# Performance work log

Measured on AMD Instinct MI355X. Metric: run time of the kernel, lower is better.

The kernel has to match this reference:

```python
import jax, jax.numpy as jnp
import numpy as np

R_MAX = 32
S_MAX = 2
N_RES_BINS = 2 * R_MAX + 2      # 66 (shared by residue and token one-hots)
N_CHAIN_BINS = 2 * S_MAX + 2    # 6
NO_BINS = N_RES_BINS + N_RES_BINS + 1 + N_CHAIN_BINS  # 139
C_Z = 128


def setup_inputs() -> dict:
    key = jax.random.key(0)
    ks = jax.random.split(key, 6)
    B, N = 1, 1024
    asym_id = jax.random.randint(ks[0], (B, N), 0, 8, dtype=jnp.int32)
    residue_index = jnp.sort(jax.random.randint(ks[1], (B, N), 0, 1024, dtype=jnp.int32), axis=-1)
    entity_id = jax.random.randint(ks[2], (B, N), 0, 4, dtype=jnp.int32)
    token_index = jnp.sort(jax.random.randint(ks[3], (B, N), 0, 2048, dtype=jnp.int32), axis=-1)
    sym_id = jax.random.randint(ks[4], (B, N), 0, 4, dtype=jnp.int32)
    # Linear(no_bins, c_z, bias=False): weight shape [c_z, no_bins]
    W = jax.random.normal(ks[5], (C_Z, NO_BINS), dtype=jnp.float32) * (NO_BINS ** -0.5)
    return {
        "asym_id": asym_id,
        "residue_index": residue_index,
        "entity_id": entity_id,
        "token_index": token_index,
        "sym_id": sym_id,
        "W": W,
    }


def _rel_feat(asym_id, residue_index, entity_id, token_index, sym_id, dtype=jnp.float32):
    # pairwise [B, N, N] comparisons
    b_same_chain = asym_id[..., :, None] == asym_id[..., None, :]
    b_same_residue = residue_index[..., :, None] == residue_index[..., None, :]
    b_same_entity = entity_id[..., :, None] == entity_id[..., None, :]

    # residue-level relative position, clamped; off-chain -> sentinel bin 2*r_max+1
    d_residue = residue_index[..., :, None] - residue_index[..., None, :]
    d_residue = jnp.clip(d_residue + R_MAX, 0, 2 * R_MAX)
    d_residue = jnp.where(b_same_chain, d_residue, 2 * R_MAX + 1)
    a_rel_pos = jax.nn.one_hot(d_residue, N_RES_BINS, dtype=dtype)

    # token-level relative position within same chain & residue
    d_token = token_index[..., :, None] - token_index[..., None, :]
    d_token = jnp.clip(d_token + R_MAX, 0, 2 * R_MAX)
    d_token = jnp.where(b_same_chain & b_same_residue, d_token, 2 * R_MAX + 1)
    a_rel_token = jax.nn.one_hot(d_token, N_RES_BINS, dtype=dtype)

    # chain-level relative position within same entity
    d_chain = sym_id[..., :, None] - sym_id[..., None, :]
    d_chain = jnp.clip(d_chain + S_MAX, 0, 2 * S_MAX)
    d_chain = jnp.where(b_same_entity, d_chain, 2 * S_MAX + 1)
    a_rel_chain = jax.nn.one_hot(d_chain, N_CHAIN_BINS, dtype=dtype)

    # [B, N, N, no_bins]
    return jnp.concatenate(
        [a_rel_pos, a_rel_token, b_same_entity[..., None].astype(dtype), a_rel_chain],
        axis=-1,
    )


def reference(asym_id, residue_index, entity_id, token_index, sym_id, W):
    rel_feat = _rel_feat(asym_id, residue_index, entity_id, token_index, sym_id, W.dtype)
    # bias-free Linear: rel_feat @ W^T -> [B, N, N, c_z]
    return jnp.einsum('...b,cb->...c', rel_feat, W)
```

## Files before the change

### kernel.cpp

```cpp
#include <hip/hip_runtime.h>


#define R_MAX 32
#define NO_BINS 139
#define C_Z 128
#define C_HALF 64
#define N_MAX 1024
#define WSTRIDE 68

typedef float v4f __attribute__((ext_vector_type(4)));

__global__ __launch_bounds__(256) void relpos_kernel(
    const int* __restrict__ asym, const int* __restrict__ res,
    const int* __restrict__ ent,  const int* __restrict__ tok,
    const int* __restrict__ sym,  const float* __restrict__ W,
    float* __restrict__ out, int N)
{
    __shared__ float wt[NO_BINS * WSTRIDE];
    __shared__ int   jb_pack[N_MAX];

    const int tid   = threadIdx.x;
    const int c_off = blockIdx.x * C_HALF;
    const int i     = blockIdx.y;

    const float* __restrict__ Wr = W + (size_t)c_off * NO_BINS;
    for (int q = tid; q < (C_HALF * NO_BINS) / 4; q += 256) {
        const v4f v = *(const v4f*)(Wr + 4 * q);
        const int e = 4 * q;
#pragma unroll
        for (int k = 0; k < 4; ++k) {
            const int ee = e + k;
            const int c  = ee / NO_BINS;
            const int b  = ee - c * NO_BINS;
            wt[b * WSTRIDE + c] = v[k];
        }
    }

    const int ai = asym[i], ri = res[i], ei = ent[i], ti = tok[i], si = sym[i];

    for (int j = tid; j < N; j += 256) {
        const int rj = res[j], tj = tok[j], aj = asym[j], ej = ent[j], sj = sym[j];
        const bool sc  = (ai == aj);
        const bool sr  = (ri == rj);
        const bool seB = (ei == ej);

        int dr = min(max(ri - rj + R_MAX, 0), 2 * R_MAX);
        if (!sc) dr = 2 * R_MAX + 1;
        int dt = min(max(ti - tj + R_MAX, 0), 2 * R_MAX);
        if (!(sc && sr)) dt = 2 * R_MAX + 1;
        int dc = min(max(si - sj + 2, 0), 4);
        if (!seB) dc = 5;

        jb_pack[j] = dr | ((66 + dt) << 7) | ((133 + dc) << 15) | ((seB ? 1 : 0) << 23);
    }
    __syncthreads();

    const int c4 = (tid & 15) * 4;
    const int jl = tid >> 4;

    const v4f entv = *(const v4f*)&wt[132 * WSTRIDE + c4];

    float* po = out + ((size_t)i * N + jl) * C_Z + c_off + c4;

    for (int jb = 0; jb < N; jb += 16) {
        const int pk   = jb_pack[jb + jl];
        const int rowR = pk & 127;
        const int rowT = (pk >> 7) & 255;
        const int rowC = (pk >> 15) & 255;
        const float se = (pk >> 23) ? 1.0f : 0.0f;

        const v4f r0 = *(const v4f*)&wt[rowR * WSTRIDE + c4];
        const v4f t0 = *(const v4f*)&wt[rowT * WSTRIDE + c4];
        const v4f k0 = *(const v4f*)&wt[rowC * WSTRIDE + c4];

        v4f o;
        o.x = fmaf(se, entv.x, r0.x + t0.x + k0.x);
        o.y = fmaf(se, entv.y, r0.y + t0.y + k0.y);
        o.z = fmaf(se, entv.z, r0.z + t0.z + k0.z);
        o.w = fmaf(se, entv.w, r0.w + t0.w + k0.w);

        __builtin_nontemporal_store(o, (v4f*)po);
        po += 16 * C_Z;
    }
}

extern "C" void kernel_launch(void* const* d_in, const int* in_sizes, int n_in,
                              void* d_out, int out_size, void* d_ws, size_t ws_size,
                              hipStream_t stream) {
    const int*   asym = (const int*)d_in[0];
    const int*   res  = (const int*)d_in[1];
    const int*   ent  = (const int*)d_in[2];
    const int*   tok  = (const int*)d_in[3];
    const int*   sym  = (const int*)d_in[4];
    const float* W    = (const float*)d_in[5];
    float* out = (float*)d_out;

    const int N = in_sizes[0];
    dim3 grid(C_Z / C_HALF, N);
    relpos_kernel<<<grid, 256, 0, stream>>>(asym, res, ent, tok, sym, W, out, N);
}
```

Before: 530.7 us.

## Process two rows per block over all channels to amortize weight staging

Each block now covers the full 128 channels and two query rows i, instead of half the channels for one row. It also uses 512 threads and stages the whole transposed weight table in LDS once per block. This halves the total weight-staging work and removes the per-block redundancy across channel halves. The cost is a larger LDS footprint (about 73KB), which may cap occupancy, plus extra barriers to rebuild the packed index table for each row.

After: 532.8 us. Within noise of the previous version (+0.4%).

```diff
diff --git a/kernel.cpp b/kernel.cpp
--- a/kernel.cpp
+++ b/kernel.cpp
@@ -4,13 +4,31 @@
 #define R_MAX 32
 #define NO_BINS 139
 #define C_Z 128
-#define C_HALF 64
 #define N_MAX 1024
-#define WSTRIDE 68
+#define WSTRIDE 132
+#define NI 2
+#define NTHREADS 512
 
 typedef float v4f __attribute__((ext_vector_type(4)));
 
-__global__ __launch_bounds__(256) void relpos_kernel(
+__device__ __forceinline__ int make_pack(int ai, int ri, int ei, int ti, int si,
+                                         int aj, int rj, int ej, int tj, int sj)
+{
+    const bool sc = (ai == aj);
+    const bool sr = (ri == rj);
+    const bool se = (ei == ej);
+
+    int dr = min(max(ri - rj + R_MAX, 0), 2 * R_MAX);
+    if (!sc) dr = 2 * R_MAX + 1;
+    int dt = min(max(ti - tj + R_MAX, 0), 2 * R_MAX);
+    if (!(sc && sr)) dt = 2 * R_MAX + 1;
+    int dc = min(max(si - sj + 2, 0), 4);
+    if (!se) dc = 5;
+
+    return dr | ((66 + dt) << 7) | ((133 + dc) << 15) | ((se ? 1 : 0) << 23);
+}
+
+__global__ __launch_bounds__(NTHREADS) void relpos_kernel(
     const int* __restrict__ asym, const int* __restrict__ res,
     const int* __restrict__ ent,  const int* __restrict__ tok,
     const int* __restrict__ sym,  const float* __restrict__ W,
@@ -19,13 +37,11 @@
     __shared__ float wt[NO_BINS * WSTRIDE];
     __shared__ int   jb_pack[N_MAX];
 
-    const int tid   = threadIdx.x;
-    const int c_off = blockIdx.x * C_HALF;
-    const int i     = blockIdx.y;
+    const int tid = threadIdx.x;
+    const int i0  = blockIdx.x * NI;
 
-    const float* __restrict__ Wr = W + (size_t)c_off * NO_BINS;
-    for (int q = tid; q < (C_HALF * NO_BINS) / 4; q += 256) {
-        const v4f v = *(const v4f*)(Wr + 4 * q);
+    for (int q = tid; q < (C_Z * NO_BINS) / 4; q += NTHREADS) {
+        const v4f v = *(const v4f*)(W + 4 * q);
         const int e = 4 * q;
 #pragma unroll
         for (int k = 0; k < 4; ++k) {
@@ -36,51 +52,52 @@
         }
     }
 
-    const int ai = asym[i], ri = res[i], ei = ent[i], ti = tok[i], si = sym[i];
+    const int j0 = tid, j1 = tid + NTHREADS;
+    const int rj0 = res[j0], tj0 = tok[j0], aj0 = asym[j0],
+              ej0 = ent[j0], sj0 = sym[j0];
+    int rj1 = 0, tj1 = 0, aj1 = 0, ej1 = 0, sj1 = 0;
+    const bool has1 = (j1 < N);
+    if (has1) { rj1 = res[j1]; tj1 = tok[j1]; aj1 = asym[j1];
+                ej1 = ent[j1]; sj1 = sym[j1]; }
 
-    for (int j = tid; j < N; j += 256) {
-        const int rj = res[j], tj = tok[j], aj = asym[j], ej = ent[j], sj = sym[j];
-        const bool sc  = (ai == aj);
-        const bool sr  = (ri == rj);
-        const bool seB = (ei == ej);
+    const int c4 = (tid & 31) * 4;
+    const int jl = tid >> 5;
 
-        int dr = min(max(ri - rj + R_MAX, 0), 2 * R_MAX);
-        if (!sc) dr = 2 * R_MAX + 1;
-        int dt = min(max(ti - tj + R_MAX, 0), 2 * R_MAX);
-        if (!(sc && sr)) dt = 2 * R_MAX + 1;
-        int dc = min(max(si - sj + 2, 0), 4);
-        if (!seB) dc = 5;
+    for (int ii = 0; ii < NI; ++ii) {
+        const int i = i0 + ii;
+        if (i >= N) break;
 
-        jb_pack[j] = dr | ((66 + dt) << 7) | ((133 + dc) << 15) | ((seB ? 1 : 0) << 23);
-    }
-    __syncthreads();
+        const int ai = asym[i], ri = res[i], ei = ent[i], ti = tok[i], si = sym[i];
 
-    const int c4 = (tid & 15) * 4;
-    const int jl = tid >> 4;
+        __syncthreads();
+        jb_pack[j0] = make_pack(ai, ri, ei, ti, si, aj0, rj0, ej0, tj0, sj0);
+        if (has1)
+            jb_pack[j1] = make_pack(ai, ri, ei, ti, si, aj1, rj1, ej1, tj1, sj1);
+        __syncthreads();
 
-    const v4f entv = *(const v4f*)&wt[132 * WSTRIDE + c4];
+        const v4f entv = *(const v4f*)&wt[132 * WSTRIDE + c4];
+        float* po = out + ((size_t)i * N + jl) * C_Z + c4;
 
-    float* po = out + ((size_t)i * N + jl) * C_Z + c_off + c4;
+        for (int jb = 0; jb < N; jb += 16) {
+            const int pk   = jb_pack[jb + jl];
+            const int rowR = pk & 127;
+            const int rowT = (pk >> 7) & 255;
+            const int rowC = (pk >> 15) & 255;
+            const float se = (pk >> 23) ? 1.0f : 0.0f;
 
-    for (int jb = 0; jb < N; jb += 16) {
-        const int pk   = jb_pack[jb + jl];
-        const int rowR = pk & 127;
-        const int rowT = (pk >> 7) & 255;
-        const int rowC = (pk >> 15) & 255;
-        const float se = (pk >> 23) ? 1.0f : 0.0f;
+            const v4f r0 = *(const v4f*)&wt[rowR * WSTRIDE + c4];
+            const v4f t0 = *(const v4f*)&wt[rowT * WSTRIDE + c4];
+            const v4f k0 = *(const v4f*)&wt[rowC * WSTRIDE + c4];
 
-        const v4f r0 = *(const v4f*)&wt[rowR * WSTRIDE + c4];
-        const v4f t0 = *(const v4f*)&wt[rowT * WSTRIDE + c4];
-        const v4f k0 = *(const v4f*)&wt[rowC * WSTRIDE + c4];
+            v4f o;
+            o.x = fmaf(se, entv.x, r0.x + t0.x + k0.x);
+            o.y = fmaf(se, entv.y, r0.y + t0.y + k0.y);
+            o.z = fmaf(se, entv.z, r0.z + t0.z + k0.z);
+            o.w = fmaf(se, entv.w, r0.w + t0.w + k0.w);
 
-        v4f o;
-        o.x = fmaf(se, entv.x, r0.x + t0.x + k0.x);
-        o.y = fmaf(se, entv.y, r0.y + t0.y + k0.y);
-        o.z = fmaf(se, entv.z, r0.z + t0.z + k0.z);
-        o.w = fmaf(se, entv.w, r0.w + t0.w + k0.w);
-
-        __builtin_nontemporal_store(o, (v4f*)po);
-        po += 16 * C_Z;
+            __builtin_nontemporal_store(o, (v4f*)po);
+            po += 16 * C_Z;
+        }
     }
 }
 
@@ -96,6 +113,6 @@
     float* out = (float*)d_out;
 
     const int N = in_sizes[0];
-    dim3 grid(C_Z / C_HALF, N);
-    relpos_kernel<<<grid, 256, 0, stream>>>(asym, res, ent, tok, sym, W, out, N);
+    dim3 grid((N + NI - 1) / NI);
+    relpos_kernel<<<grid, NTHREADS, 0, stream>>>(asym, res, ent, tok, sym, W, out, N);
 }
```
